# Performance work log

Hardware: AMD Instinct MI355X
Metric: run time of the kernel (lower is better)

Reference implementation:

```python
import jax, jax.numpy as jnp
import numpy as np

NUM_BATCH = 16  # B: number of point clouds in the ragged batch
NUM_POINTS = 500000  # N: total points across the batch
NUM_TRANS = 128  # M*B: stacked SE3 transforms (num_multi = 8)


def setup_inputs() -> dict:
    key = jax.random.key(0)
    k1, k2, k3 = jax.random.split(key, 3)
    trans = jax.random.normal(k1, (NUM_TRANS, 4, 4), dtype=jnp.float32)
    xyz = jax.random.normal(k2, (NUM_POINTS, 3), dtype=jnp.float32)
    batch = jax.random.randint(k3, (NUM_POINTS,), 0, NUM_BATCH, dtype=jnp.int32)
    # guarantee batch.max() + 1 == NUM_BATCH (matches the module's assert)
    batch = batch.at[:NUM_BATCH].set(jnp.arange(NUM_BATCH, dtype=jnp.int32))
    return {"trans": trans, "xyz": xyz, "batch": batch}


def reference(trans, xyz, batch):
    """SE3Transform.forward (PARTIAL_DENSE path) == multi_partial_transform.

    trans: [M*B, 4, 4], xyz: [N, 3], batch: [N] in [0, B).
    Returns (new_pos [M*N, 3], new_batch [M*N]).
    The original's per-batch Python loop with boolean masks is expressed as a
    single fused gather + per-point affine: out_i = R[nb_i] @ x_i + p[nb_i].
    """
    B = NUM_BATCH
    M = trans.shape[0] // B
    N = xyz.shape[0]
    # replicate points M times, offset batch ids per replica
    offs = (jnp.arange(M, dtype=batch.dtype) * B)[:, None]  # [M,1]
    new_batch = (batch[None, :] + offs).reshape(-1)  # [M*N]
    xyz_rep = jnp.broadcast_to(xyz[None], (M, N, 3)).reshape(-1, 3)  # [M*N,3]
    R = trans[new_batch, :3, :3]  # [M*N,3,3]
    p = trans[new_batch, :3, 3]   # [M*N,3]
    new_pos = jnp.einsum('nij,nj->ni', R, xyz_rep) + p
    return new_pos, new_batch
```

## Files before the change

### kernel.cpp

```cpp
#include <hip/hip_runtime.h>


#define NPTS   500000
#define POSF4  375000
#define BATF4  125000
#define NT     128
#define TSTR   20

typedef float f32x4 __attribute__((ext_vector_type(4)));

__device__ __forceinline__ void nt_store4(float4 v, float4* p) {
    f32x4 w; w.x = v.x; w.y = v.y; w.z = v.z; w.w = v.w;
    __builtin_nontemporal_store(w, (f32x4*)p);
}

__global__ __launch_bounds__(256) void se3_kernel(
    const float* __restrict__ trans,
    const float* __restrict__ xyz,
    const int*   __restrict__ batch,
    float* __restrict__ out)
{
    __shared__ float s_t[NT * TSTR];

    const int tid = threadIdx.x;
    const int F   = blockIdx.x * 256;
    const int t   = F + tid;

    if (F < POSF4) {
        for (int i = tid; i < NT * 4; i += 256) {
            int pt = i >> 2, row = i & 3;
            float4 v = ((const float4*)trans)[i];
            *(float4*)&s_t[pt * TSTR + row * 4] = v;
        }
        __syncthreads();
    }

    if (t < POSF4) {
        const int f  = t;
        const int t3 = f % 3;
        const int w  = 4 * f - t3;
        const int n0 = w / 3;

        const int a0 = w & ~3;
        const float4 v0 = *(const float4*)(xyz + a0);
        const float4 v1 = *(const float4*)(xyz + a0 + 4);
        const float  d8 = xyz[t3 == 1 ? a0 + 8 : a0];

        const float xa = t3 == 0 ? v0.x : (t3 == 1 ? v0.w : v0.z);
        const float xb = t3 == 0 ? v0.y : (t3 == 1 ? v1.x : v0.w);
        const float xc = t3 == 0 ? v0.z : (t3 == 1 ? v1.y : v1.x);
        const float xd = t3 == 0 ? v0.w : (t3 == 1 ? v1.z : v1.y);
        const float xe = t3 == 0 ? v1.x : (t3 == 1 ? v1.w : v1.z);
        const float xf = t3 == 0 ? v1.y : (t3 == 1 ? d8   : v1.w);

        const int b0 = batch[n0];
        const int b1 = batch[n0 + 1];

        int   ro[4];
        float X0[4], X1[4], X2[4];
        #pragma unroll
        for (int k = 0; k < 4; ++k) {
            int ck = t3 + k, sel = 0;
            if (ck >= 3) { ck -= 3; sel = 1; }
            int b = sel ? b1 : b0;
            ro[k] = b * (TSTR * 4) + ck * 16;
            X0[k] = sel ? xd : xa;
            X1[k] = sel ? xe : xb;
            X2[k] = sel ? xf : xc;
        }

        const char* stb = (const char*)s_t;
        float4* po = (float4*)out;
        #pragma unroll
        for (int m = 0; m < 8; ++m) {
            float4 r0 = *(const float4*)(stb + ro[0] + m * 1280);
            float4 r1 = *(const float4*)(stb + ro[1] + m * 1280);
            float4 r2 = *(const float4*)(stb + ro[2] + m * 1280);
            float4 r3 = *(const float4*)(stb + ro[3] + m * 1280);
            float4 v;
            v.x = fmaf(r0.x, X0[0], fmaf(r0.y, X1[0], fmaf(r0.z, X2[0], r0.w)));
            v.y = fmaf(r1.x, X0[1], fmaf(r1.y, X1[1], fmaf(r1.z, X2[1], r1.w)));
            v.z = fmaf(r2.x, X0[2], fmaf(r2.y, X1[2], fmaf(r2.z, X2[2], r2.w)));
            v.w = fmaf(r3.x, X0[3], fmaf(r3.y, X1[3], fmaf(r3.z, X2[3], r3.w)));
            nt_store4(v, &po[m * POSF4 + f]);
        }
    } else if (t < POSF4 + BATF4) {
        const int q = t - POSF4;
        int4 b4 = ((const int4*)batch)[q];
        float4* ob = (float4*)(out + 12000000);
        #pragma unroll
        for (int m = 0; m < 8; ++m) {
            const int a = m * 16;
            float4 v = make_float4((float)(b4.x + a), (float)(b4.y + a),
                                   (float)(b4.z + a), (float)(b4.w + a));
            nt_store4(v, &ob[m * BATF4 + q]);
        }
    }
}

extern "C" void kernel_launch(void* const* d_in, const int* in_sizes, int n_in,
                              void* d_out, int out_size, void* d_ws, size_t ws_size,
                              hipStream_t stream) {
    const float* trans = (const float*)d_in[0];
    const float* xyz   = (const float*)d_in[1];
    const int*   batch = (const int*)d_in[2];
    float* out = (float*)d_out;

    const int total = POSF4 + BATF4;
    const int block = 256;
    const int grid  = (total + block - 1) / block;
    se3_kernel<<<grid, block, 0, stream>>>(trans, xyz, batch, out);
}
```

Measured before the change: 85.48 us.

## Split replicas across two blocks, hoist global loads, drop nontemporal stores

```diff
diff --git a/kernel.cpp b/kernel.cpp
--- a/kernel.cpp
+++ b/kernel.cpp
@@ -4,15 +4,7 @@
 #define NPTS   500000
 #define POSF4  375000
 #define BATF4  125000
-#define NT     128
 #define TSTR   20
-
-typedef float f32x4 __attribute__((ext_vector_type(4)));
-
-__device__ __forceinline__ void nt_store4(float4 v, float4* p) {
-    f32x4 w; w.x = v.x; w.y = v.y; w.z = v.z; w.w = v.w;
-    __builtin_nontemporal_store(w, (f32x4*)p);
-}
 
 __global__ __launch_bounds__(256) void se3_kernel(
     const float* __restrict__ trans,
@@ -20,41 +12,50 @@
     const int*   __restrict__ batch,
     float* __restrict__ out)
 {
-    __shared__ float s_t[NT * TSTR];
+    __shared__ float s_t[64 * TSTR];
 
-    const int tid = threadIdx.x;
-    const int F   = blockIdx.x * 256;
-    const int t   = F + tid;
+    const int tid   = threadIdx.x;
+    const int bx    = blockIdx.x;
+    const int chunk = bx >> 1;
+    const int mh    = bx & 1;
+    const int F     = chunk * 256;
+    const int t     = F + tid;
+
+    const bool isPos = t < POSF4;
+
+    float4 v0, v1; float d8 = 0.f; int b0 = 0, b1 = 0, t3 = 0;
+    v0 = make_float4(0.f, 0.f, 0.f, 0.f); v1 = v0;
+    if (isPos) {
+        const int f  = t;
+        t3 = f % 3;
+        const int w  = 4 * f - t3;
+        const int n0 = w / 3;
+        const int a0 = w & ~3;
+        v0 = *(const float4*)(xyz + a0);
+        v1 = *(const float4*)(xyz + a0 + 4);
+        d8 = xyz[t3 == 1 ? a0 + 8 : a0];
+        b0 = batch[n0];
+        b1 = batch[n0 + 1];
+    }
 
     if (F < POSF4) {
-        for (int i = tid; i < NT * 4; i += 256) {
-            int pt = i >> 2, row = i & 3;
-            float4 v = ((const float4*)trans)[i];
+        {
+            const int i = tid;
+            const int pt = i >> 2, row = i & 3;
+            float4 v = ((const float4*)trans)[256 * mh + i];
             *(float4*)&s_t[pt * TSTR + row * 4] = v;
         }
         __syncthreads();
     }
 
-    if (t < POSF4) {
-        const int f  = t;
-        const int t3 = f % 3;
-        const int w  = 4 * f - t3;
-        const int n0 = w / 3;
-
-        const int a0 = w & ~3;
-        const float4 v0 = *(const float4*)(xyz + a0);
-        const float4 v1 = *(const float4*)(xyz + a0 + 4);
-        const float  d8 = xyz[t3 == 1 ? a0 + 8 : a0];
-
+    if (isPos) {
+        const int f = t;
         const float xa = t3 == 0 ? v0.x : (t3 == 1 ? v0.w : v0.z);
         const float xb = t3 == 0 ? v0.y : (t3 == 1 ? v1.x : v0.w);
         const float xc = t3 == 0 ? v0.z : (t3 == 1 ? v1.y : v1.x);
         const float xd = t3 == 0 ? v0.w : (t3 == 1 ? v1.z : v1.y);
         const float xe = t3 == 0 ? v1.x : (t3 == 1 ? v1.w : v1.z);
         const float xf = t3 == 0 ? v1.y : (t3 == 1 ? d8   : v1.w);
-
-        const int b0 = batch[n0];
-        const int b1 = batch[n0 + 1];
 
         int   ro[4];
         float X0[4], X1[4], X2[4];
@@ -72,28 +73,29 @@
         const char* stb = (const char*)s_t;
         float4* po = (float4*)out;
         #pragma unroll
-        for (int m = 0; m < 8; ++m) {
-            float4 r0 = *(const float4*)(stb + ro[0] + m * 1280);
-            float4 r1 = *(const float4*)(stb + ro[1] + m * 1280);
-            float4 r2 = *(const float4*)(stb + ro[2] + m * 1280);
-            float4 r3 = *(const float4*)(stb + ro[3] + m * 1280);
+        for (int mm = 0; mm < 4; ++mm) {
+            const int m = 4 * mh + mm;
+            float4 r0 = *(const float4*)(stb + ro[0] + mm * 1280);
+            float4 r1 = *(const float4*)(stb + ro[1] + mm * 1280);
+            float4 r2 = *(const float4*)(stb + ro[2] + mm * 1280);
+            float4 r3 = *(const float4*)(stb + ro[3] + mm * 1280);
             float4 v;
             v.x = fmaf(r0.x, X0[0], fmaf(r0.y, X1[0], fmaf(r0.z, X2[0], r0.w)));
             v.y = fmaf(r1.x, X0[1], fmaf(r1.y, X1[1], fmaf(r1.z, X2[1], r1.w)));
             v.z = fmaf(r2.x, X0[2], fmaf(r2.y, X1[2], fmaf(r2.z, X2[2], r2.w)));
             v.w = fmaf(r3.x, X0[3], fmaf(r3.y, X1[3], fmaf(r3.z, X2[3], r3.w)));
-            nt_store4(v, &po[m * POSF4 + f]);
+            po[m * POSF4 + f] = v;
         }
     } else if (t < POSF4 + BATF4) {
         const int q = t - POSF4;
         int4 b4 = ((const int4*)batch)[q];
         float4* ob = (float4*)(out + 12000000);
         #pragma unroll
-        for (int m = 0; m < 8; ++m) {
+        for (int mm = 0; mm < 4; ++mm) {
+            const int m = 4 * mh + mm;
             const int a = m * 16;
-            float4 v = make_float4((float)(b4.x + a), (float)(b4.y + a),
-                                   (float)(b4.z + a), (float)(b4.w + a));
-            nt_store4(v, &ob[m * BATF4 + q]);
+            ob[m * BATF4 + q] = make_float4((float)(b4.x + a), (float)(b4.y + a),
+                                            (float)(b4.z + a), (float)(b4.w + a));
         }
     }
 }
@@ -108,6 +110,7 @@
 
     const int total = POSF4 + BATF4;
     const int block = 256;
-    const int grid  = (total + block - 1) / block;
+    const int chunks = (total + block - 1) / block;
+    const int grid   = 2 * chunks;
     se3_kernel<<<grid, block, 0, stream>>>(trans, xyz, batch, out);
 }
```

After: 84.33 us. About the same (-1.3%).
